# Performance work log

Hardware: AMD Instinct MI355X
Metric: run time of the kernel (lower is better)

Reference implementation:

```python
import jax, jax.numpy as jnp
import numpy as np

K = 32          # init k
E = 0.003       # EMA rate e


def setup_inputs() -> dict:
    key = jax.random.key(0)
    k1, _ = jax.random.split(key)
    features = jax.random.normal(k1, (512, 6, 8192), dtype=jnp.float32)
    threshold = jnp.zeros((1,), dtype=jnp.float32)
    return {"features": features, "threshold": threshold}


def reference(features, threshold):
    batch_size, n_layers, d_features = features.shape
    batch_k = K * batch_size * n_layers
    flat = features.reshape(-1)                      # [B*L*D]
    topk_vals, topk_idxs = jax.lax.top_k(flat, batch_k)
    topk_vals = jax.nn.relu(topk_vals)
    out = jnp.zeros_like(flat).at[topk_idxs].set(topk_vals)
    out = out.reshape(batch_size, n_layers, d_features)
    min_k = jax.lax.stop_gradient(jnp.min(topk_vals))
    new_threshold = (1.0 - E) * threshold + E * min_k
    return out, new_threshold
```

## Files before the change

### kernel.cpp

```cpp
#include <hip/hip_runtime.h>
#include <stdint.h>

#define K_TOTAL   98304u
#define EMA_RATE  0.003f

#define SBINS      4096
#define SSHIFT     20
#define SAMPLE_V4  16384
#define STARGET    640u

#define CBINS      4096
#define CSHIFT     12
#define CAP2       16384u
#define OCAP       65536u
#define EQCAP      256

#define MP_BLOCKS  1024
#define MP_THREADS 256
#define MP_U       24
#define NWAVES     4096
#define WCAP       256

__device__ __forceinline__ unsigned f2key(float x) {
    unsigned u = __float_as_uint(x);
    return (u & 0x80000000u) ? ~u : (u | 0x80000000u);
}
__device__ __forceinline__ float key2f(unsigned key) {
    unsigned u = (key & 0x80000000u) ? (key & 0x7FFFFFFFu) : ~key;
    return __uint_as_float(u);
}


__global__ __launch_bounds__(256) void sample_hist_kernel(
        const float4* __restrict__ in, unsigned* __restrict__ shist) {
    __shared__ unsigned h[SBINS];
    for (int i = threadIdx.x; i < SBINS; i += 256) h[i] = 0;
    __syncthreads();
    unsigned s0 = blockIdx.x * 512 + threadIdx.x;
    #pragma unroll
    for (int u = 0; u < 2; ++u) {
        float4 v = in[s0 + u * 256];
        atomicAdd(&h[f2key(v.x) >> SSHIFT], 1u);
        atomicAdd(&h[f2key(v.y) >> SSHIFT], 1u);
        atomicAdd(&h[f2key(v.z) >> SSHIFT], 1u);
        atomicAdd(&h[f2key(v.w) >> SSHIFT], 1u);
    }
    __syncthreads();
    for (int i = threadIdx.x; i < SBINS; i += 256) {
        unsigned c = h[i];
        if (c) atomicAdd(&shist[i], c);
    }
}

__global__ __launch_bounds__(256) void sample_scan_kernel(
        const unsigned* __restrict__ shist, unsigned* __restrict__ ctrs) {
    __shared__ unsigned psum[256];
    const int GB = SBINS / 256;
    int t = threadIdx.x;
    int hi = SBINS - 1 - t * GB;
    unsigned c[GB];
    #pragma unroll
    for (int j = 0; j < GB; ++j) c[j] = shist[hi - j];
    unsigned s = 0;
    #pragma unroll
    for (int j = 0; j < GB; ++j) s += c[j];
    psum[t] = s;
    __syncthreads();
    for (int off = 1; off < 256; off <<= 1) {
        unsigned o = (t >= off) ? psum[t - off] : 0u;
        __syncthreads();
        psum[t] += o;
        __syncthreads();
    }
    unsigned cum = psum[t] - s;
    for (int j = 0; j < GB; ++j) {
        if (cum < STARGET && cum + c[j] >= STARGET) {
            unsigned bin = (unsigned)(hi - j);
            unsigned bb = (bin > 0) ? bin - 1 : 0;
            ctrs[2] = bb << SSHIFT;
        }
        cum += c[j];
    }
}

__global__ __launch_bounds__(MP_THREADS) void main_pass_kernel(
        const float4* __restrict__ in, unsigned* __restrict__ ctrs,
        uint2* __restrict__ wreg, unsigned* __restrict__ wcnt,
        uint2* __restrict__ ovf) {
    const unsigned gtid = blockIdx.x * MP_THREADS + threadIdx.x;
    const unsigned nth  = MP_BLOCKS * MP_THREADS;
    float thresh = key2f(ctrs[2]);

    float4 v[MP_U];
    #pragma unroll
    for (int u = 0; u < MP_U; ++u) v[u] = in[gtid + u * nth];
    __builtin_amdgcn_sched_barrier(0);

    unsigned gw = gtid >> 6;
    uint2* wb = wreg + (size_t)gw * WCAP;
    unsigned wcount = 0;
    #pragma unroll
    for (int u = 0; u < MP_U; ++u) {
        float xs[4] = {v[u].x, v[u].y, v[u].z, v[u].w};
        #pragma unroll
        for (int c = 0; c < 4; ++c) {
            bool pred = xs[c] >= thresh;
            unsigned long long mask = __ballot(pred);
            if (mask) {
                if (pred) {
                    unsigned prefix = __builtin_amdgcn_mbcnt_hi(
                        (unsigned)(mask >> 32),
                        __builtin_amdgcn_mbcnt_lo((unsigned)mask, 0u));
                    unsigned off = wcount + prefix;
                    unsigned idx = 4u * (gtid + u * nth) + c;
                    if (off < WCAP) {
                        wb[off] = make_uint2(f2key(xs[c]), idx);
                    } else {
                        unsigned q = atomicAdd(&ctrs[0], 1u);
                        if (q < OCAP) ovf[q] = make_uint2(f2key(xs[c]), idx);
                    }
                }
                wcount += (unsigned)__popcll(mask);
            }
        }
    }
    if ((threadIdx.x & 63u) == 0)
        wcnt[gw] = (wcount < WCAP) ? wcount : WCAP;
}

__global__ __launch_bounds__(256) void cand_hist_kernel(
        const uint2* __restrict__ wreg, const unsigned* __restrict__ wcnt,
        const uint2* __restrict__ ovf, const unsigned* __restrict__ ctrs,
        unsigned* __restrict__ ghist) {
    __shared__ unsigned h[CBINS];
    for (int i = threadIdx.x; i < CBINS; i += 256) h[i] = 0;
    __syncthreads();
    unsigned base = ctrs[2];
    unsigned tid = blockIdx.x * 256 + threadIdx.x;
    unsigned nth = gridDim.x * 256;
    const unsigned NSLOT = NWAVES * WCAP;
    for (unsigned s = tid; s < NSLOT; s += nth) {
        unsigned w = s >> 8;
        if ((s & 255u) < wcnt[w]) {
            unsigned g = (wreg[s].x - base) >> CSHIFT;
            if (g > CBINS - 1) g = CBINS - 1;
            atomicAdd(&h[g], 1u);
        }
    }
    unsigned no = min(ctrs[0], (unsigned)OCAP);
    for (unsigned s = tid; s < no; s += nth) {
        unsigned g = (ovf[s].x - base) >> CSHIFT;
        if (g > CBINS - 1) g = CBINS - 1;
        atomicAdd(&h[g], 1u);
    }
    __syncthreads();
    for (int i = threadIdx.x; i < CBINS; i += 256) {
        unsigned c = h[i];
        if (c) atomicAdd(&ghist[i], c);
    }
}

__global__ __launch_bounds__(256) void find_g_kernel(
        const unsigned* __restrict__ ghist, unsigned* __restrict__ ctrs) {
    __shared__ unsigned psum[256];
    const int GB = CBINS / 256;
    int t = threadIdx.x;
    int hi = CBINS - 1 - t * GB;
    unsigned c[GB];
    #pragma unroll
    for (int j = 0; j < GB; ++j) c[j] = ghist[hi - j];
    unsigned s = 0;
    #pragma unroll
    for (int j = 0; j < GB; ++j) s += c[j];
    psum[t] = s;
    __syncthreads();
    for (int off = 1; off < 256; off <<= 1) {
        unsigned o = (t >= off) ? psum[t - off] : 0u;
        __syncthreads();
        psum[t] += o;
        __syncthreads();
    }
    unsigned cum = psum[t] - s;
    for (int j = 0; j < GB; ++j) {
        if (cum < K_TOTAL && cum + c[j] >= K_TOTAL) {
            ctrs[3] = (unsigned)(hi - j);
            ctrs[4] = K_TOTAL - cum;
        }
        cum += c[j];
    }
}

__global__ __launch_bounds__(256) void scatter_kernel(
        const uint2* __restrict__ wreg, const unsigned* __restrict__ wcnt,
        const uint2* __restrict__ ovf, unsigned* __restrict__ ctrs,
        unsigned* __restrict__ kval2, unsigned* __restrict__ cidx2,
        float* __restrict__ out) {
    unsigned base  = ctrs[2];
    unsigned gstar = ctrs[3];
    unsigned tid = blockIdx.x * 256 + threadIdx.x;
    unsigned nth = gridDim.x * 256;
    const unsigned NSLOT = NWAVES * WCAP;
    for (unsigned s = tid; s < NSLOT; s += nth) {
        unsigned w = s >> 8;
        if ((s & 255u) < wcnt[w]) {
            uint2 e = wreg[s];
            unsigned g = (e.x - base) >> CSHIFT;
            if (g > CBINS - 1) g = CBINS - 1;
            if (g > gstar) {
                out[e.y] = fmaxf(key2f(e.x), 0.0f);
            } else if (g == gstar) {
                unsigned p = atomicAdd(&ctrs[1], 1u);
                if (p < CAP2) { kval2[p] = e.x; cidx2[p] = e.y; }
            }
        }
    }
    unsigned no = min(ctrs[0], (unsigned)OCAP);
    for (unsigned s = tid; s < no; s += nth) {
        uint2 e = ovf[s];
        unsigned g = (e.x - base) >> CSHIFT;
        if (g > CBINS - 1) g = CBINS - 1;
        if (g > gstar) {
            out[e.y] = fmaxf(key2f(e.x), 0.0f);
        } else if (g == gstar) {
            unsigned p = atomicAdd(&ctrs[1], 1u);
            if (p < CAP2) { kval2[p] = e.x; cidx2[p] = e.y; }
        }
    }
}

__global__ __launch_bounds__(256) void final_kernel(
        const unsigned* __restrict__ kval2, const unsigned* __restrict__ cidx2,
        const unsigned* __restrict__ ctrs, float* __restrict__ out,
        const float* __restrict__ thr_in, float* __restrict__ thr_out) {
    __shared__ unsigned h[1 << CSHIFT];
    __shared__ unsigned psum[256];
    __shared__ unsigned eqidx[EQCAP];
    __shared__ unsigned eqcnt;
    __shared__ unsigned sh_low, sh_need3;
    const int NB = 1 << CSHIFT;
    int t = threadIdx.x;
    unsigned nc2   = min(ctrs[1], (unsigned)CAP2);
    unsigned base3 = ctrs[2] + (ctrs[3] << CSHIFT);
    unsigned need2 = ctrs[4];

    for (int i = t; i < NB; i += 256) h[i] = 0;
    if (t == 0) eqcnt = 0;
    __syncthreads();
    for (unsigned i = t; i < nc2; i += 256) {
        unsigned low = kval2[i] - base3;
        if (low > (unsigned)(NB - 1)) low = NB - 1;
        atomicAdd(&h[low], 1u);
    }
    __syncthreads();

    const int GB = NB / 256;
    int hi = NB - 1 - t * GB;
    unsigned s = 0;
    for (int j = 0; j < GB; ++j) s += h[hi - j];
    psum[t] = s;
    __syncthreads();
    for (int off = 1; off < 256; off <<= 1) {
        unsigned o = (t >= off) ? psum[t - off] : 0u;
        __syncthreads();
        psum[t] += o;
        __syncthreads();
    }
    unsigned cum = psum[t] - s;
    for (int j = 0; j < GB; ++j) {
        unsigned c = h[hi - j];
        if (cum < need2 && cum + c >= need2) {
            sh_low = (unsigned)(hi - j);
            sh_need3 = need2 - cum;
        }
        cum += c;
    }
    __syncthreads();
    unsigned kth_key = base3 + sh_low;
    unsigned need3   = sh_need3;

    for (unsigned i = t; i < nc2; i += 256) {
        unsigned key = kval2[i];
        if (key > kth_key) {
            out[cidx2[i]] = fmaxf(key2f(key), 0.0f);
        } else if (key == kth_key) {
            unsigned p = atomicAdd(&eqcnt, 1u);
            if (p < EQCAP) eqidx[p] = cidx2[i];
        }
    }
    __syncthreads();

    unsigned ne = min(eqcnt, (unsigned)EQCAP);
    float vv = key2f(kth_key);
    for (unsigned e = t; e < ne; e += 256) {
        unsigned my = eqidx[e];
        unsigned rank = 0;
        for (unsigned f = 0; f < ne; ++f) rank += (eqidx[f] < my) ? 1u : 0u;
        if (rank < need3) out[my] = fmaxf(vv, 0.0f);
    }

    if (t == 0) {
        float mink = fmaxf(vv, 0.0f);
        thr_out[0] = (1.0f - EMA_RATE) * thr_in[0] + EMA_RATE * mink;
    }
}

extern "C" void kernel_launch(void* const* d_in, const int* in_sizes, int n_in,
                              void* d_out, int out_size, void* d_ws, size_t ws_size,
                              hipStream_t stream) {
    const float4* feat   = (const float4*)d_in[0];
    const float*  thr_in = (const float*)d_in[1];
    float* out = (float*)d_out;
    int N = in_sizes[0];

    uint8_t* w = (uint8_t*)d_ws;
    unsigned* shist = (unsigned*)w;
    unsigned* ghist = (unsigned*)(w + (16 << 10));
    unsigned* ctrs  = (unsigned*)(w + (32 << 10));
    unsigned* wcnt  = (unsigned*)(w + (36 << 10));
    uint2*    wreg  = (uint2*)(w + ((size_t)1 << 20));
    uint2*    ovf   = (uint2*)(w + ((size_t)10 << 20));
    unsigned* kval2 = (unsigned*)(w + ((size_t)11 << 20));
    unsigned* cidx2 = (unsigned*)(w + ((size_t)11 << 20) + CAP2 * 4);

    hipMemsetAsync(d_ws, 0, (32 << 10) + 64, stream);
    hipMemsetAsync(d_out, 0, (size_t)N * 4, stream);

    sample_hist_kernel<<<32,  256, 0, stream>>>(feat, shist);
    sample_scan_kernel<<<1,   256, 0, stream>>>(shist, ctrs);
    main_pass_kernel  <<<MP_BLOCKS, MP_THREADS, 0, stream>>>(feat, ctrs,
                                                             wreg, wcnt, ovf);
    cand_hist_kernel  <<<128, 256, 0, stream>>>(wreg, wcnt, ovf, ctrs, ghist);
    find_g_kernel     <<<1,   256, 0, stream>>>(ghist, ctrs);
    scatter_kernel    <<<128, 256, 0, stream>>>(wreg, wcnt, ovf, ctrs,
                                                kval2, cidx2, out);
    final_kernel      <<<1,   256, 0, stream>>>(kval2, cidx2, ctrs,
                                                out, thr_in, out + N);
}
```

Before: 245.4 us.

## Fuse top-k pipeline into three kernels with last-block reductions

Merges the sample histogram and scan into a single one-block kernel that also zeroes the workspace, removing a memset and a launch. Candidate histogramming moves into the main pass, and a last-block-done atomic counter runs the bucket search there. The scatter and final refine are fused the same way, and candidate key/index pairs are packed into 64-bit stores. Main-pass geometry changes to more blocks with fewer loads per thread and a smaller per-wave buffer. This trades launch overhead and an extra pass over the candidates for atomic fences and a serial tail in the last block, and it risks more overflow with the smaller buffer and sample.

```diff
diff --git a/kernel.cpp b/kernel.cpp
--- a/kernel.cpp
+++ b/kernel.cpp
@@ -6,8 +6,9 @@
 
 #define SBINS      4096
 #define SSHIFT     20
-#define SAMPLE_V4  16384
-#define STARGET    640u
+#define S_THREADS  1024
+#define S_V4       8192
+#define STARGET    320u
 
 #define CBINS      4096
 #define CSHIFT     12
@@ -15,11 +16,12 @@
 #define OCAP       65536u
 #define EQCAP      256
 
-#define MP_BLOCKS  1024
+#define MP_BLOCKS  3072
 #define MP_THREADS 256
-#define MP_U       24
-#define NWAVES     4096
-#define WCAP       256
+#define MP_U       8
+#define NWAVES     (MP_BLOCKS * MP_THREADS / 64)
+#define WCAP       128
+
 
 __device__ __forceinline__ unsigned f2key(float x) {
     unsigned u = __float_as_uint(x);
@@ -29,44 +31,44 @@
     unsigned u = (key & 0x80000000u) ? (key & 0x7FFFFFFFu) : ~key;
     return __uint_as_float(u);
 }
-
-
-__global__ __launch_bounds__(256) void sample_hist_kernel(
-        const float4* __restrict__ in, unsigned* __restrict__ shist) {
+__device__ __forceinline__ unsigned aload(const unsigned* p) {
+    return __hip_atomic_load(p, __ATOMIC_RELAXED, __HIP_MEMORY_SCOPE_AGENT);
+}
+
+__global__ __launch_bounds__(S_THREADS) void sample_kernel(
+        const float4* __restrict__ in, unsigned* __restrict__ ctrs,
+        unsigned* __restrict__ ghist) {
     __shared__ unsigned h[SBINS];
-    for (int i = threadIdx.x; i < SBINS; i += 256) h[i] = 0;
-    __syncthreads();
-    unsigned s0 = blockIdx.x * 512 + threadIdx.x;
-    #pragma unroll
-    for (int u = 0; u < 2; ++u) {
-        float4 v = in[s0 + u * 256];
-        atomicAdd(&h[f2key(v.x) >> SSHIFT], 1u);
-        atomicAdd(&h[f2key(v.y) >> SSHIFT], 1u);
-        atomicAdd(&h[f2key(v.z) >> SSHIFT], 1u);
-        atomicAdd(&h[f2key(v.w) >> SSHIFT], 1u);
-    }
-    __syncthreads();
-    for (int i = threadIdx.x; i < SBINS; i += 256) {
-        unsigned c = h[i];
-        if (c) atomicAdd(&shist[i], c);
-    }
-}
-
-__global__ __launch_bounds__(256) void sample_scan_kernel(
-        const unsigned* __restrict__ shist, unsigned* __restrict__ ctrs) {
-    __shared__ unsigned psum[256];
-    const int GB = SBINS / 256;
+    __shared__ unsigned psum[S_THREADS];
     int t = threadIdx.x;
+    for (int i = t; i < SBINS; i += S_THREADS) h[i] = 0;
+    for (int i = t; i < CBINS; i += S_THREADS) ghist[i] = 0;
+    if (t < 16) ctrs[t] = 0;
+    __syncthreads();
+
+    float4 v[8];
+    #pragma unroll
+    for (int u = 0; u < 8; ++u) v[u] = in[t + u * S_THREADS];
+    #pragma unroll
+    for (int u = 0; u < 8; ++u) {
+        atomicAdd(&h[f2key(v[u].x) >> SSHIFT], 1u);
+        atomicAdd(&h[f2key(v[u].y) >> SSHIFT], 1u);
+        atomicAdd(&h[f2key(v[u].z) >> SSHIFT], 1u);
+        atomicAdd(&h[f2key(v[u].w) >> SSHIFT], 1u);
+    }
+    __syncthreads();
+
+    const int GB = SBINS / S_THREADS;
     int hi = SBINS - 1 - t * GB;
     unsigned c[GB];
     #pragma unroll
-    for (int j = 0; j < GB; ++j) c[j] = shist[hi - j];
+    for (int j = 0; j < GB; ++j) c[j] = h[hi - j];
     unsigned s = 0;
     #pragma unroll
     for (int j = 0; j < GB; ++j) s += c[j];
     psum[t] = s;
     __syncthreads();
-    for (int off = 1; off < 256; off <<= 1) {
+    for (int off = 1; off < S_THREADS; off <<= 1) {
         unsigned o = (t >= off) ? psum[t - off] : 0u;
         __syncthreads();
         psum[t] += o;
@@ -86,10 +88,17 @@
 __global__ __launch_bounds__(MP_THREADS) void main_pass_kernel(
         const float4* __restrict__ in, unsigned* __restrict__ ctrs,
         uint2* __restrict__ wreg, unsigned* __restrict__ wcnt,
-        uint2* __restrict__ ovf) {
-    const unsigned gtid = blockIdx.x * MP_THREADS + threadIdx.x;
+        uint2* __restrict__ ovf, unsigned* __restrict__ ghist) {
+    __shared__ unsigned h[CBINS];
+    __shared__ unsigned psum[MP_THREADS];
+    __shared__ unsigned sh_last;
+    const unsigned t = threadIdx.x;
+    for (int i = t; i < CBINS; i += MP_THREADS) h[i] = 0;
+    const unsigned gtid = blockIdx.x * MP_THREADS + t;
     const unsigned nth  = MP_BLOCKS * MP_THREADS;
-    float thresh = key2f(ctrs[2]);
+    unsigned base = ctrs[2];
+    float thresh = key2f(base);
+    __syncthreads();
 
     float4 v[MP_U];
     #pragma unroll
@@ -108,73 +117,55 @@
             unsigned long long mask = __ballot(pred);
             if (mask) {
                 if (pred) {
+                    unsigned key = f2key(xs[c]);
+                    unsigned g = (key - base) >> CSHIFT;
+                    if (g > CBINS - 1) g = CBINS - 1;
+                    atomicAdd(&h[g], 1u);
                     unsigned prefix = __builtin_amdgcn_mbcnt_hi(
                         (unsigned)(mask >> 32),
                         __builtin_amdgcn_mbcnt_lo((unsigned)mask, 0u));
                     unsigned off = wcount + prefix;
                     unsigned idx = 4u * (gtid + u * nth) + c;
                     if (off < WCAP) {
-                        wb[off] = make_uint2(f2key(xs[c]), idx);
+                        wb[off] = make_uint2(key, idx);
                     } else {
                         unsigned q = atomicAdd(&ctrs[0], 1u);
-                        if (q < OCAP) ovf[q] = make_uint2(f2key(xs[c]), idx);
+                        if (q < OCAP) ovf[q] = make_uint2(key, idx);
                     }
                 }
                 wcount += (unsigned)__popcll(mask);
             }
         }
     }
-    if ((threadIdx.x & 63u) == 0)
-        wcnt[gw] = (wcount < WCAP) ? wcount : WCAP;
-}
-
-__global__ __launch_bounds__(256) void cand_hist_kernel(
-        const uint2* __restrict__ wreg, const unsigned* __restrict__ wcnt,
-        const uint2* __restrict__ ovf, const unsigned* __restrict__ ctrs,
-        unsigned* __restrict__ ghist) {
-    __shared__ unsigned h[CBINS];
-    for (int i = threadIdx.x; i < CBINS; i += 256) h[i] = 0;
-    __syncthreads();
-    unsigned base = ctrs[2];
-    unsigned tid = blockIdx.x * 256 + threadIdx.x;
-    unsigned nth = gridDim.x * 256;
-    const unsigned NSLOT = NWAVES * WCAP;
-    for (unsigned s = tid; s < NSLOT; s += nth) {
-        unsigned w = s >> 8;
-        if ((s & 255u) < wcnt[w]) {
-            unsigned g = (wreg[s].x - base) >> CSHIFT;
-            if (g > CBINS - 1) g = CBINS - 1;
-            atomicAdd(&h[g], 1u);
-        }
-    }
-    unsigned no = min(ctrs[0], (unsigned)OCAP);
-    for (unsigned s = tid; s < no; s += nth) {
-        unsigned g = (ovf[s].x - base) >> CSHIFT;
-        if (g > CBINS - 1) g = CBINS - 1;
-        atomicAdd(&h[g], 1u);
-    }
-    __syncthreads();
-    for (int i = threadIdx.x; i < CBINS; i += 256) {
+    if ((t & 63u) == 0) wcnt[gw] = (wcount < WCAP) ? wcount : WCAP;
+    __syncthreads();
+    for (int i = t; i < CBINS; i += MP_THREADS) {
         unsigned c = h[i];
         if (c) atomicAdd(&ghist[i], c);
     }
-}
-
-__global__ __launch_bounds__(256) void find_g_kernel(
-        const unsigned* __restrict__ ghist, unsigned* __restrict__ ctrs) {
-    __shared__ unsigned psum[256];
-    const int GB = CBINS / 256;
-    int t = threadIdx.x;
+    __syncthreads();
+
+    if (t == 0) {
+        __threadfence();
+        unsigned prev = __hip_atomic_fetch_add(&ctrs[5], 1u,
+                            __ATOMIC_ACQ_REL, __HIP_MEMORY_SCOPE_AGENT);
+        sh_last = (prev == gridDim.x - 1) ? 1u : 0u;
+    }
+    __syncthreads();
+    if (!sh_last) return;
+    __threadfence();
+
+    const int GB = CBINS / MP_THREADS;
     int hi = CBINS - 1 - t * GB;
     unsigned c[GB];
     #pragma unroll
-    for (int j = 0; j < GB; ++j) c[j] = ghist[hi - j];
+    for (int j = 0; j < GB; ++j) c[j] = aload(&ghist[hi - j]);
     unsigned s = 0;
     #pragma unroll
     for (int j = 0; j < GB; ++j) s += c[j];
     psum[t] = s;
     __syncthreads();
-    for (int off = 1; off < 256; off <<= 1) {
+    for (int off = 1; off < MP_THREADS; off <<= 1) {
         unsigned o = (t >= off) ? psum[t - off] : 0u;
         __syncthreads();
         psum[t] += o;
@@ -190,19 +181,27 @@
     }
 }
 
-__global__ __launch_bounds__(256) void scatter_kernel(
+#define SF_BLOCKS 256
+__global__ __launch_bounds__(256) void scatter_final_kernel(
         const uint2* __restrict__ wreg, const unsigned* __restrict__ wcnt,
         const uint2* __restrict__ ovf, unsigned* __restrict__ ctrs,
-        unsigned* __restrict__ kval2, unsigned* __restrict__ cidx2,
-        float* __restrict__ out) {
+        unsigned long long* __restrict__ kc2, float* __restrict__ out,
+        const float* __restrict__ thr_in, float* __restrict__ thr_out) {
+    __shared__ unsigned h[CBINS];
+    __shared__ unsigned psum[256];
+    __shared__ unsigned eqidx[EQCAP];
+    __shared__ unsigned eqcnt;
+    __shared__ unsigned sh_low, sh_need3, sh_last;
+    const unsigned t = threadIdx.x;
     unsigned base  = ctrs[2];
     unsigned gstar = ctrs[3];
-    unsigned tid = blockIdx.x * 256 + threadIdx.x;
-    unsigned nth = gridDim.x * 256;
+    unsigned tid = blockIdx.x * 256 + t;
+    unsigned nth = SF_BLOCKS * 256;
     const unsigned NSLOT = NWAVES * WCAP;
+
     for (unsigned s = tid; s < NSLOT; s += nth) {
-        unsigned w = s >> 8;
-        if ((s & 255u) < wcnt[w]) {
+        unsigned w = s >> 7;
+        if ((s & 127u) < wcnt[w]) {
             uint2 e = wreg[s];
             unsigned g = (e.x - base) >> CSHIFT;
             if (g > CBINS - 1) g = CBINS - 1;
@@ -210,11 +209,16 @@
                 out[e.y] = fmaxf(key2f(e.x), 0.0f);
             } else if (g == gstar) {
                 unsigned p = atomicAdd(&ctrs[1], 1u);
-                if (p < CAP2) { kval2[p] = e.x; cidx2[p] = e.y; }
+                if (p < CAP2) {
+                    unsigned long long pk =
+                        ((unsigned long long)e.y << 32) | e.x;
+                    __hip_atomic_store(&kc2[p], pk, __ATOMIC_RELAXED,
+                                       __HIP_MEMORY_SCOPE_AGENT);
+                }
             }
         }
     }
-    unsigned no = min(ctrs[0], (unsigned)OCAP);
+    unsigned no = min(aload(&ctrs[0]), (unsigned)OCAP);
     for (unsigned s = tid; s < no; s += nth) {
         uint2 e = ovf[s];
         unsigned g = (e.x - base) >> CSHIFT;
@@ -223,31 +227,37 @@
             out[e.y] = fmaxf(key2f(e.x), 0.0f);
         } else if (g == gstar) {
             unsigned p = atomicAdd(&ctrs[1], 1u);
-            if (p < CAP2) { kval2[p] = e.x; cidx2[p] = e.y; }
-        }
-    }
-}
-
-__global__ __launch_bounds__(256) void final_kernel(
-        const unsigned* __restrict__ kval2, const unsigned* __restrict__ cidx2,
-        const unsigned* __restrict__ ctrs, float* __restrict__ out,
-        const float* __restrict__ thr_in, float* __restrict__ thr_out) {
-    __shared__ unsigned h[1 << CSHIFT];
-    __shared__ unsigned psum[256];
-    __shared__ unsigned eqidx[EQCAP];
-    __shared__ unsigned eqcnt;
-    __shared__ unsigned sh_low, sh_need3;
+            if (p < CAP2) {
+                unsigned long long pk = ((unsigned long long)e.y << 32) | e.x;
+                __hip_atomic_store(&kc2[p], pk, __ATOMIC_RELAXED,
+                                   __HIP_MEMORY_SCOPE_AGENT);
+            }
+        }
+    }
+    __syncthreads();
+
+    if (t == 0) {
+        __threadfence();
+        unsigned prev = __hip_atomic_fetch_add(&ctrs[6], 1u,
+                            __ATOMIC_ACQ_REL, __HIP_MEMORY_SCOPE_AGENT);
+        sh_last = (prev == gridDim.x - 1) ? 1u : 0u;
+    }
+    __syncthreads();
+    if (!sh_last) return;
+    __threadfence();
+
+    unsigned nc2   = min(aload(&ctrs[1]), (unsigned)CAP2);
+    unsigned base3 = base + (gstar << CSHIFT);
+    unsigned need2 = ctrs[4];
     const int NB = 1 << CSHIFT;
-    int t = threadIdx.x;
-    unsigned nc2   = min(ctrs[1], (unsigned)CAP2);
-    unsigned base3 = ctrs[2] + (ctrs[3] << CSHIFT);
-    unsigned need2 = ctrs[4];
 
     for (int i = t; i < NB; i += 256) h[i] = 0;
     if (t == 0) eqcnt = 0;
     __syncthreads();
     for (unsigned i = t; i < nc2; i += 256) {
-        unsigned low = kval2[i] - base3;
+        unsigned long long pk = __hip_atomic_load(&kc2[i], __ATOMIC_RELAXED,
+                                                  __HIP_MEMORY_SCOPE_AGENT);
+        unsigned low = (unsigned)pk - base3;
         if (low > (unsigned)(NB - 1)) low = NB - 1;
         atomicAdd(&h[low], 1u);
     }
@@ -279,12 +289,15 @@
     unsigned need3   = sh_need3;
 
     for (unsigned i = t; i < nc2; i += 256) {
-        unsigned key = kval2[i];
+        unsigned long long pk = __hip_atomic_load(&kc2[i], __ATOMIC_RELAXED,
+                                                  __HIP_MEMORY_SCOPE_AGENT);
+        unsigned key = (unsigned)pk;
+        unsigned idx = (unsigned)(pk >> 32);
         if (key > kth_key) {
-            out[cidx2[i]] = fmaxf(key2f(key), 0.0f);
+            out[idx] = fmaxf(key2f(key), 0.0f);
         } else if (key == kth_key) {
             unsigned p = atomicAdd(&eqcnt, 1u);
-            if (p < EQCAP) eqidx[p] = cidx2[i];
+            if (p < EQCAP) eqidx[p] = idx;
         }
     }
     __syncthreads();
@@ -313,26 +326,18 @@
     int N = in_sizes[0];
 
     uint8_t* w = (uint8_t*)d_ws;
-    unsigned* shist = (unsigned*)w;
-    unsigned* ghist = (unsigned*)(w + (16 << 10));
-    unsigned* ctrs  = (unsigned*)(w + (32 << 10));
-    unsigned* wcnt  = (unsigned*)(w + (36 << 10));
-    uint2*    wreg  = (uint2*)(w + ((size_t)1 << 20));
-    uint2*    ovf   = (uint2*)(w + ((size_t)10 << 20));
-    unsigned* kval2 = (unsigned*)(w + ((size_t)11 << 20));
-    unsigned* cidx2 = (unsigned*)(w + ((size_t)11 << 20) + CAP2 * 4);
-
-    hipMemsetAsync(d_ws, 0, (32 << 10) + 64, stream);
+    unsigned*           ghist = (unsigned*)w;
+    unsigned*           ctrs  = (unsigned*)(w + (16 << 10));
+    unsigned*           wcnt  = (unsigned*)(w + (20 << 10));
+    uint2*              wreg  = (uint2*)(w + ((size_t)1 << 20));
+    uint2*              ovf   = (uint2*)(w + ((size_t)14 << 20));
+    unsigned long long* kc2   = (unsigned long long*)(w + ((size_t)15 << 20));
+
     hipMemsetAsync(d_out, 0, (size_t)N * 4, stream);
 
-    sample_hist_kernel<<<32,  256, 0, stream>>>(feat, shist);
-    sample_scan_kernel<<<1,   256, 0, stream>>>(shist, ctrs);
-    main_pass_kernel  <<<MP_BLOCKS, MP_THREADS, 0, stream>>>(feat, ctrs,
-                                                             wreg, wcnt, ovf);
-    cand_hist_kernel  <<<128, 256, 0, stream>>>(wreg, wcnt, ovf, ctrs, ghist);
-    find_g_kernel     <<<1,   256, 0, stream>>>(ghist, ctrs);
-    scatter_kernel    <<<128, 256, 0, stream>>>(wreg, wcnt, ovf, ctrs,
-                                                kval2, cidx2, out);
-    final_kernel      <<<1,   256, 0, stream>>>(kval2, cidx2, ctrs,
-                                                out, thr_in, out + N);
-}
+    sample_kernel       <<<1, S_THREADS, 0, stream>>>(feat, ctrs, ghist);
+    main_pass_kernel    <<<MP_BLOCKS, MP_THREADS, 0, stream>>>(
+        feat, ctrs, wreg, wcnt, ovf, ghist);
+    scatter_final_kernel<<<SF_BLOCKS, 256, 0, stream>>>(
+        wreg, wcnt, ovf, ctrs, kc2, out, thr_in, out + N);
+}
```

Measured after the change: 465.5 us. 1.9x slower.
